# Kernel optimization log

Hardware: AMD Instinct MI355X
Metric: run time of the kernel (lower is better)

The kernel has to match this reference:

```python
import jax, jax.numpy as jnp
import numpy as np

CH_IN = 256
CA = CH_IN // 8   # attention channels (theta/phi)
CH = CH_IN // 2   # value channels (g)


def _maxpool2(t):
    # 2x2 max pool, stride 2: (B,C,H,W) -> (B,C,H//2,W//2)
    b, c, h, w = t.shape
    return t.reshape(b, c, h // 2, 2, w // 2, 2).max(axis=(3, 5))


def setup_inputs() -> dict:
    key = jax.random.key(0)
    ks = jax.random.split(key, 6)
    B, H, W = 16, 64, 64
    x = jax.random.normal(ks[0], (B, CH_IN, H, W), dtype=jnp.float32)
    # 1x1 conv weights stored as (out_ch, in_ch); spectral_norm is a weight
    # reparameterization, so the forward math is a plain conv with these weights.
    s = 0.05
    w_theta = jax.random.normal(ks[1], (CA, CH_IN), dtype=jnp.float32) * s
    w_phi = jax.random.normal(ks[2], (CA, CH_IN), dtype=jnp.float32) * s
    w_g = jax.random.normal(ks[3], (CH, CH_IN), dtype=jnp.float32) * s
    w_o = jax.random.normal(ks[4], (CH_IN, CH), dtype=jnp.float32) * s
    # gamma is initialized to 0 in the module; use a nonzero value so the
    # attention branch contributes to the output.
    gamma = jnp.asarray(0.5, dtype=jnp.float32)
    return {"x": x, "w_theta": w_theta, "w_phi": w_phi, "w_g": w_g,
            "w_o": w_o, "gamma": gamma}


def reference(x, w_theta, w_phi, w_g, w_o, gamma):
    B, C, H, W = x.shape
    # 1x1 convs as channel contractions
    theta = jnp.einsum('oc,bchw->bohw', w_theta, x)            # (B,CA,H,W)
    phi = _maxpool2(jnp.einsum('oc,bchw->bohw', w_phi, x))     # (B,CA,H/2,W/2)
    g = _maxpool2(jnp.einsum('oc,bchw->bohw', w_g, x))         # (B,CH,H/2,W/2)
    N = H * W
    M = N // 4
    theta = theta.reshape(B, CA, N)
    phi = phi.reshape(B, CA, M)
    g = g.reshape(B, CH, M)
    # beta = softmax(theta^T phi) over keys (no scaling, as in original)
    beta = jax.nn.softmax(jnp.einsum('bcn,bcm->bnm', theta, phi), axis=-1)  # (B,N,M)
    o = jnp.einsum('bcm,bnm->bcn', g, beta).reshape(B, CH, H, W)
    o = jnp.einsum('oc,bchw->bohw', w_o, o)                    # (B,C,H,W)
    return gamma * o + x
```

## Files before the change

kernel.cpp:

```cpp
#include <hip/hip_runtime.h>
#include <hip/hip_bf16.h>

#define NB 16
#define CIN 256
#define CA 32
#define CH 128
#define NN 4096
#define MM 1024

typedef __attribute__((ext_vector_type(8))) short s16x8;
typedef __attribute__((ext_vector_type(4))) float f32x4;

static __device__ __forceinline__ unsigned short f2bf(float x) {
  __hip_bfloat16 h = __float2bfloat16(x);
  return __builtin_bit_cast(unsigned short, h);
}
static __device__ __forceinline__ float bf2f(unsigned short u) {
  unsigned int v = ((unsigned int)u) << 16;
  return __builtin_bit_cast(float, v);
}
static __device__ __forceinline__ unsigned int pk2(float a, float b) {
  return (unsigned)f2bf(a) | ((unsigned)f2bf(b) << 16);
}
static __device__ __forceinline__ unsigned int pk2t(float a, float b) {
  return (__builtin_bit_cast(unsigned int, a) >> 16) |
         (__builtin_bit_cast(unsigned int, b) & 0xffff0000u);
}
static __device__ __forceinline__ void gload_lds16(const void* g, void* s) {
  __builtin_amdgcn_global_load_lds(
      (const __attribute__((address_space(1))) unsigned int*)g,
      (__attribute__((address_space(3))) unsigned int*)s, 16, 0, 0);
}

__global__ __launch_bounds__(256) void k_wcvt(const float* __restrict__ w_theta,
                                              const float* __restrict__ w_phi,
                                              const float* __restrict__ w_g,
                                              const float* __restrict__ w_o,
                                              unsigned short* __restrict__ wcat2,
                                              unsigned short* __restrict__ wo2) {
  const int i = blockIdx.x * 256 + threadIdx.x;
  if (i < 49152) {
    const int row = i >> 8, c = i & 255;
    const float v = (row < 32) ? w_theta[i]
                  : (row < 64) ? w_phi[i - 8192]
                               : w_g[i - 16384];
    const int dst = ((row >> 4) * 8 + (c >> 5)) * 512 +
                    (((c >> 3) & 3) * 16 + (row & 15)) * 8 + (c & 7);
    wcat2[dst] = f2bf(v);
  } else {
    const int w = i - 49152;
    const int c_out = w >> 7, k = w & 127;
    const int grp = (k >> 2) & 3;
    const int j = (((k >> 4) & 1) << 2) | (k & 3);
    const int dst = ((c_out >> 4) * 16 + (k >> 5) * 4 + grp) * 128 +
                    ((c_out & 15) << 3) + j;
    wo2[dst] = f2bf(w_o[w]);
  }
}

__global__ __launch_bounds__(512) void k_proj(const float* __restrict__ x,
                                              const unsigned short* __restrict__ wcat2,
                                              unsigned short* __restrict__ theta,
                                              unsigned short* __restrict__ phi2,
                                              unsigned short* __restrict__ g2) {
  __shared__ unsigned short lds[192 * 136];
  unsigned short (*xl)[32][132] = reinterpret_cast<unsigned short(*)[32][132]>(lds);
  unsigned short (*ol)[136] = reinterpret_cast<unsigned short(*)[136]>(lds);
  const int b = blockIdx.y;
  const int t = blockIdx.x;
  const int tid = threadIdx.x;
  const int wv = tid >> 6;
  const int l = tid & 63;
  const int grp = l >> 4, col = l & 15;
  const float* xb = x + (size_t)b * CIN * NN;
  const int cl0 = tid >> 5, nq0 = tid & 31;
  const int cl1 = (tid + 512) >> 5, nq1 = tid & 31;
  float4 ra0, ra1;
  auto LOADX = [&](int kc) {
    ra0 = *reinterpret_cast<const float4*>(xb + (size_t)(kc * 32 + cl0) * NN + t * 128 + nq0 * 4);
    ra1 = *reinterpret_cast<const float4*>(xb + (size_t)(kc * 32 + cl1) * NN + t * 128 + nq1 * 4);
  };
  auto WRITEX = [&](int buf) {
    *reinterpret_cast<uint2*>(&xl[buf][cl0][nq0 * 4]) =
        make_uint2(pk2(ra0.x, ra0.y), pk2(ra0.z, ra0.w));
    *reinterpret_cast<uint2*>(&xl[buf][cl1][nq1 * 4]) =
        make_uint2(pk2(ra1.x, ra1.y), pk2(ra1.z, ra1.w));
  };
  f32x4 acc[12];
#pragma unroll
  for (int r = 0; r < 12; ++r) acc[r] = f32x4{0.f, 0.f, 0.f, 0.f};
  LOADX(0);
  WRITEX(0);
  LOADX(1);
#pragma unroll 1
  for (int kc = 0; kc < 8; ++kc) {
    __syncthreads();
    if (kc < 7) {
      WRITEX((kc + 1) & 1);
      if (kc < 6) LOADX(kc + 2);
    }
    const int cur = kc & 1;
    s16x8 bfrag;
#pragma unroll
    for (int j = 0; j < 8; ++j)
      bfrag[j] = (short)xl[cur][grp * 8 + j][wv * 16 + col];
#pragma unroll
    for (int r = 0; r < 12; ++r) {
      const s16x8 af = *reinterpret_cast<const s16x8*>(
          wcat2 + (size_t)(r * 8 + kc) * 512 + l * 8);
      acc[r] = __builtin_amdgcn_mfma_f32_16x16x32_bf16(af, bfrag, acc[r], 0, 0, 0);
    }
  }
  __syncthreads();
#pragma unroll
  for (int r = 0; r < 12; ++r)
#pragma unroll
    for (int q = 0; q < 4; ++q)
      ol[r * 16 + grp * 4 + q][wv * 16 + col] = f2bf(acc[r][q]);
  __syncthreads();
  unsigned short* thb = theta + (size_t)b * NN * CA;
  for (int i = tid; i < 128 * 16; i += 512) {
    const int n = i >> 4, cp = (i & 15) << 1;
    const unsigned int v = (unsigned)ol[cp][n] | ((unsigned)ol[cp + 1][n] << 16);
    *reinterpret_cast<unsigned int*>(thb + (size_t)(t * 128 + n) * CA + cp) = v;
  }
  unsigned short* phb2 = phi2 + (size_t)b * MM * CA;
  for (int i = tid; i < 32 * 32; i += 512) {
    const int ca = i & 31, mx = i >> 5;
    const float v = fmaxf(
        fmaxf(bf2f(ol[32 + ca][2 * mx]), bf2f(ol[32 + ca][2 * mx + 1])),
        fmaxf(bf2f(ol[32 + ca][64 + 2 * mx]), bf2f(ol[32 + ca][64 + 2 * mx + 1])));
    const int m = t * 32 + mx;
    phb2[(m >> 4) * 512 + (ca >> 3) * 128 + (m & 15) * 8 + (ca & 7)] = f2bf(v);
  }
  unsigned short* gb2 = g2 + (size_t)b * CH * MM;
  for (int i = tid; i < 128 * 32; i += 512) {
    const int mx = i & 31, c = i >> 5;
    const float v = fmaxf(
        fmaxf(bf2f(ol[64 + c][2 * mx]), bf2f(ol[64 + c][2 * mx + 1])),
        fmaxf(bf2f(ol[64 + c][64 + 2 * mx]), bf2f(ol[64 + c][64 + 2 * mx + 1])));
    const int pg = (mx & 15) >> 2;
    const int pj = (mx & 3) | ((mx >> 4) << 2);
    gb2[(size_t)(t * 8 + (c >> 4)) * 512 + pg * 128 + (c & 15) * 8 + pj] = f2bf(v);
  }
}

__global__ __launch_bounds__(512, 4) void k_attn_out(
    const unsigned short* __restrict__ theta, const unsigned short* __restrict__ phi2,
    const unsigned short* __restrict__ g2, const unsigned short* __restrict__ wo2,
    const float* __restrict__ x, const float* __restrict__ gammap,
    float* __restrict__ out) {
  __shared__ __align__(16) unsigned short kv[2][10240];
  const int b = blockIdx.y;
  const int tid = threadIdx.x;
  const int wv = tid >> 6;
  const int l = tid & 63;
  const int grp = l >> 4, col = l & 15;
  const int n0 = blockIdx.x * 128 + wv * 16;
  const unsigned short* thb = theta + (size_t)b * NN * CA;
  const unsigned short* ph2b = phi2 + (size_t)b * MM * CA;
  const unsigned short* gb2 = g2 + (size_t)b * CH * MM;
  const s16x8 qf = *reinterpret_cast<const s16x8*>(thb + (size_t)(n0 + col) * CA + grp * 8);

  auto STAGE = [&](int buf, int tile) {
    const int mc = tile * 64;
    const unsigned short* ksrc = ph2b + (mc >> 4) * 512;
    const unsigned short* vsrc = gb2 + (size_t)(mc >> 5) * 4096;
#pragma unroll
    for (int q = 0; q < 3; ++q) {
      const int i = wv + q * 8;
      if (i < 20) {
        const unsigned short* src = (i < 4) ? (ksrc + i * 512) : (vsrc + (size_t)(i - 4) * 512);
        gload_lds16(src + (size_t)l * 8, &kv[buf][i * 512]);
      }
    }
  };

  f32x4 oa[8];
#pragma unroll
  for (int t = 0; t < 8; ++t) oa[t] = f32x4{0.f, 0.f, 0.f, 0.f};
  float m0 = 0.f, ls = 0.f;
  const f32x4 z4 = {0.f, 0.f, 0.f, 0.f};

  STAGE(0, 0);
  __syncthreads();
#pragma unroll 1
  for (int it = 0; it < 16; ++it) {
    const int cur = it & 1;
    if (it < 15) STAGE(cur ^ 1, it + 1);
    const unsigned short* kb = &kv[cur][0];
    const unsigned short* vb = &kv[cur][2048];
    const int fo = grp * 128 + col * 8;
    const s16x8 kf0 = *reinterpret_cast<const s16x8*>(kb + 0 * 512 + fo);
    const s16x8 kf1 = *reinterpret_cast<const s16x8*>(kb + 1 * 512 + fo);
    const s16x8 kf2 = *reinterpret_cast<const s16x8*>(kb + 2 * 512 + fo);
    const s16x8 kf3 = *reinterpret_cast<const s16x8*>(kb + 3 * 512 + fo);
    f32x4 s0 = __builtin_amdgcn_mfma_f32_16x16x32_bf16(kf0, qf, z4, 0, 0, 0);
    f32x4 s1 = __builtin_amdgcn_mfma_f32_16x16x32_bf16(kf1, qf, z4, 0, 0, 0);
    f32x4 s2 = __builtin_amdgcn_mfma_f32_16x16x32_bf16(kf2, qf, z4, 0, 0, 0);
    f32x4 s3 = __builtin_amdgcn_mfma_f32_16x16x32_bf16(kf3, qf, z4, 0, 0, 0);
    if (it == 0) {
      float cm = -INFINITY;
#pragma unroll
      for (int r = 0; r < 4; ++r)
        cm = fmaxf(cm, fmaxf(fmaxf(s0[r], s1[r]), fmaxf(s2[r], s3[r])));
      cm = fmaxf(cm, __shfl_xor(cm, 16));
      cm = fmaxf(cm, __shfl_xor(cm, 32));
      m0 = cm;
    }
    float p0[4], p1[4], p2[4], p3[4];
    float cs = 0.f;
#pragma unroll
    for (int r = 0; r < 4; ++r) {
      p0[r] = __expf(s0[r] - m0);
      p1[r] = __expf(s1[r] - m0);
      p2[r] = __expf(s2[r] - m0);
      p3[r] = __expf(s3[r] - m0);
      cs += (p0[r] + p1[r]) + (p2[r] + p3[r]);
    }
    ls += cs;
    const uint4 ua = make_uint4(pk2t(p0[0], p0[1]), pk2t(p0[2], p0[3]),
                                pk2t(p1[0], p1[1]), pk2t(p1[2], p1[3]));
    const uint4 ub = make_uint4(pk2t(p2[0], p2[1]), pk2t(p2[2], p2[3]),
                                pk2t(p3[0], p3[1]), pk2t(p3[2], p3[3]));
    const s16x8 pfA = __builtin_bit_cast(s16x8, ua);
    const s16x8 pfB = __builtin_bit_cast(s16x8, ub);
#pragma unroll
    for (int t = 0; t < 8; ++t) {
      const s16x8 vfA = *reinterpret_cast<const s16x8*>(vb + t * 512 + fo);
      const s16x8 vfB = *reinterpret_cast<const s16x8*>(vb + 4096 + t * 512 + fo);
      oa[t] = __builtin_amdgcn_mfma_f32_16x16x32_bf16(vfA, pfA, oa[t], 0, 0, 0);
      oa[t] = __builtin_amdgcn_mfma_f32_16x16x32_bf16(vfB, pfB, oa[t], 0, 0, 0);
    }
    __syncthreads();
  }
  ls += __shfl_xor(ls, 16);
  ls += __shfl_xor(ls, 32);
  const float ri = 1.f / ls;
  s16x8 of[4];
#pragma unroll
  for (int ks = 0; ks < 4; ++ks) {
    const uint4 u = make_uint4(
        pk2t(oa[2 * ks][0] * ri, oa[2 * ks][1] * ri),
        pk2t(oa[2 * ks][2] * ri, oa[2 * ks][3] * ri),
        pk2t(oa[2 * ks + 1][0] * ri, oa[2 * ks + 1][1] * ri),
        pk2t(oa[2 * ks + 1][2] * ri, oa[2 * ks + 1][3] * ri));
    of[ks] = __builtin_bit_cast(s16x8, u);
  }
  const float gamma = gammap[0];
  const float* xb2 = x + (size_t)b * CIN * NN;
  float* outb = out + (size_t)b * CIN * NN;
#pragma unroll 1
  for (int t2 = 0; t2 < 16; ++t2) {
    f32x4 a2 = {0.f, 0.f, 0.f, 0.f};
#pragma unroll
    for (int ks = 0; ks < 4; ++ks) {
      const s16x8 wf = *reinterpret_cast<const s16x8*>(
          wo2 + (size_t)(t2 * 16 + ks * 4 + grp) * 128 + col * 8);
      a2 = __builtin_amdgcn_mfma_f32_16x16x32_bf16(wf, of[ks], a2, 0, 0, 0);
    }
#pragma unroll
    for (int r = 0; r < 4; ++r) {
      const size_t idx = (size_t)(t2 * 16 + grp * 4 + r) * NN + n0 + col;
      outb[idx] = fmaf(gamma, a2[r], xb2[idx]);
    }
  }
}

extern "C" void kernel_launch(void* const* d_in, const int* in_sizes, int n_in,
                              void* d_out, int out_size, void* d_ws, size_t ws_size,
                              hipStream_t stream) {
  const float* x = (const float*)d_in[0];
  const float* w_theta = (const float*)d_in[1];
  const float* w_phi = (const float*)d_in[2];
  const float* w_g = (const float*)d_in[3];
  const float* w_o = (const float*)d_in[4];
  const float* gamma = (const float*)d_in[5];
  float* out = (float*)d_out;
  char* ws = (char*)d_ws;
  unsigned short* theta = (unsigned short*)(ws + 0);
  unsigned short* phi2 = (unsigned short*)(ws + 4194304);
  unsigned short* g2 = (unsigned short*)(ws + 5242880);
  unsigned short* wo2 = (unsigned short*)(ws + 9437184);
  unsigned short* wcat2 = (unsigned short*)(ws + 9502720);

  k_wcvt<<<dim3(320), 256, 0, stream>>>(w_theta, w_phi, w_g, w_o, wcat2, wo2);
  k_proj<<<dim3(NN / 128, NB), 512, 0, stream>>>(x, wcat2, theta, phi2, g2);
  k_attn_out<<<dim3(NN / 128, NB), 512, 0, stream>>>(theta, phi2, g2, wo2, x, gamma, out);
}
```

Before: 76.02 us.

## Process two query tiles per wave to reuse staged K/V fragments

Each wave now handles 32 query rows (two 16-row MFMA tiles) instead of 16, so every K/V fragment read from LDS feeds twice as many MFMAs. The grid is halved, which cuts global K/V staging traffic per query. In exchange, accumulator registers double, launch bounds drop to 2 blocks per CU, and only 256 blocks remain, which may reduce occupancy and latency hiding.

```diff
diff --git a/kernel.cpp b/kernel.cpp
--- a/kernel.cpp
+++ b/kernel.cpp
@@ -145,7 +145,7 @@
   }
 }
 
-__global__ __launch_bounds__(512, 4) void k_attn_out(
+__global__ __launch_bounds__(512, 2) void k_attn_out(
     const unsigned short* __restrict__ theta, const unsigned short* __restrict__ phi2,
     const unsigned short* __restrict__ g2, const unsigned short* __restrict__ wo2,
     const float* __restrict__ x, const float* __restrict__ gammap,
@@ -156,11 +156,12 @@
   const int wv = tid >> 6;
   const int l = tid & 63;
   const int grp = l >> 4, col = l & 15;
-  const int n0 = blockIdx.x * 128 + wv * 16;
+  const int n0 = blockIdx.x * 256 + wv * 32;
   const unsigned short* thb = theta + (size_t)b * NN * CA;
   const unsigned short* ph2b = phi2 + (size_t)b * MM * CA;
   const unsigned short* gb2 = g2 + (size_t)b * CH * MM;
-  const s16x8 qf = *reinterpret_cast<const s16x8*>(thb + (size_t)(n0 + col) * CA + grp * 8);
+  const s16x8 qf0 = *reinterpret_cast<const s16x8*>(thb + (size_t)(n0 + col) * CA + grp * 8);
+  const s16x8 qf1 = *reinterpret_cast<const s16x8*>(thb + (size_t)(n0 + 16 + col) * CA + grp * 8);
 
   auto STAGE = [&](int buf, int tile) {
     const int mc = tile * 64;
@@ -176,10 +177,13 @@
     }
   };
 
-  f32x4 oa[8];
-#pragma unroll
-  for (int t = 0; t < 8; ++t) oa[t] = f32x4{0.f, 0.f, 0.f, 0.f};
-  float m0 = 0.f, ls = 0.f;
+  f32x4 oa0[8], oa1[8];
+#pragma unroll
+  for (int t = 0; t < 8; ++t) {
+    oa0[t] = f32x4{0.f, 0.f, 0.f, 0.f};
+    oa1[t] = f32x4{0.f, 0.f, 0.f, 0.f};
+  }
+  float m0 = 0.f, ls0 = 0.f, ls1 = 0.f;
   const f32x4 z4 = {0.f, 0.f, 0.f, 0.f};
 
   STAGE(0, 0);
@@ -195,74 +199,115 @@
     const s16x8 kf1 = *reinterpret_cast<const s16x8*>(kb + 1 * 512 + fo);
     const s16x8 kf2 = *reinterpret_cast<const s16x8*>(kb + 2 * 512 + fo);
     const s16x8 kf3 = *reinterpret_cast<const s16x8*>(kb + 3 * 512 + fo);
-    f32x4 s0 = __builtin_amdgcn_mfma_f32_16x16x32_bf16(kf0, qf, z4, 0, 0, 0);
-    f32x4 s1 = __builtin_amdgcn_mfma_f32_16x16x32_bf16(kf1, qf, z4, 0, 0, 0);
-    f32x4 s2 = __builtin_amdgcn_mfma_f32_16x16x32_bf16(kf2, qf, z4, 0, 0, 0);
-    f32x4 s3 = __builtin_amdgcn_mfma_f32_16x16x32_bf16(kf3, qf, z4, 0, 0, 0);
+    f32x4 s00 = __builtin_amdgcn_mfma_f32_16x16x32_bf16(kf0, qf0, z4, 0, 0, 0);
+    f32x4 s01 = __builtin_amdgcn_mfma_f32_16x16x32_bf16(kf1, qf0, z4, 0, 0, 0);
+    f32x4 s02 = __builtin_amdgcn_mfma_f32_16x16x32_bf16(kf2, qf0, z4, 0, 0, 0);
+    f32x4 s03 = __builtin_amdgcn_mfma_f32_16x16x32_bf16(kf3, qf0, z4, 0, 0, 0);
+    f32x4 s10 = __builtin_amdgcn_mfma_f32_16x16x32_bf16(kf0, qf1, z4, 0, 0, 0);
+    f32x4 s11 = __builtin_amdgcn_mfma_f32_16x16x32_bf16(kf1, qf1, z4, 0, 0, 0);
+    f32x4 s12 = __builtin_amdgcn_mfma_f32_16x16x32_bf16(kf2, qf1, z4, 0, 0, 0);
+    f32x4 s13 = __builtin_amdgcn_mfma_f32_16x16x32_bf16(kf3, qf1, z4, 0, 0, 0);
     if (it == 0) {
       float cm = -INFINITY;
 #pragma unroll
-      for (int r = 0; r < 4; ++r)
-        cm = fmaxf(cm, fmaxf(fmaxf(s0[r], s1[r]), fmaxf(s2[r], s3[r])));
+      for (int r = 0; r < 4; ++r) {
+        cm = fmaxf(cm, fmaxf(fmaxf(s00[r], s01[r]), fmaxf(s02[r], s03[r])));
+        cm = fmaxf(cm, fmaxf(fmaxf(s10[r], s11[r]), fmaxf(s12[r], s13[r])));
+      }
       cm = fmaxf(cm, __shfl_xor(cm, 16));
       cm = fmaxf(cm, __shfl_xor(cm, 32));
       m0 = cm;
     }
-    float p0[4], p1[4], p2[4], p3[4];
-    float cs = 0.f;
-#pragma unroll
-    for (int r = 0; r < 4; ++r) {
-      p0[r] = __expf(s0[r] - m0);
-      p1[r] = __expf(s1[r] - m0);
-      p2[r] = __expf(s2[r] - m0);
-      p3[r] = __expf(s3[r] - m0);
-      cs += (p0[r] + p1[r]) + (p2[r] + p3[r]);
-    }
-    ls += cs;
-    const uint4 ua = make_uint4(pk2t(p0[0], p0[1]), pk2t(p0[2], p0[3]),
-                                pk2t(p1[0], p1[1]), pk2t(p1[2], p1[3]));
-    const uint4 ub = make_uint4(pk2t(p2[0], p2[1]), pk2t(p2[2], p2[3]),
-                                pk2t(p3[0], p3[1]), pk2t(p3[2], p3[3]));
-    const s16x8 pfA = __builtin_bit_cast(s16x8, ua);
-    const s16x8 pfB = __builtin_bit_cast(s16x8, ub);
+    s16x8 pfA0, pfB0, pfA1, pfB1;
+    {
+      float p0[4], p1[4], p2[4], p3[4];
+      float cs = 0.f;
+#pragma unroll
+      for (int r = 0; r < 4; ++r) {
+        p0[r] = __expf(s00[r] - m0);
+        p1[r] = __expf(s01[r] - m0);
+        p2[r] = __expf(s02[r] - m0);
+        p3[r] = __expf(s03[r] - m0);
+        cs += (p0[r] + p1[r]) + (p2[r] + p3[r]);
+      }
+      ls0 += cs;
+      const uint4 ua = make_uint4(pk2t(p0[0], p0[1]), pk2t(p0[2], p0[3]),
+                                  pk2t(p1[0], p1[1]), pk2t(p1[2], p1[3]));
+      const uint4 ub = make_uint4(pk2t(p2[0], p2[1]), pk2t(p2[2], p2[3]),
+                                  pk2t(p3[0], p3[1]), pk2t(p3[2], p3[3]));
+      pfA0 = __builtin_bit_cast(s16x8, ua);
+      pfB0 = __builtin_bit_cast(s16x8, ub);
+    }
+    {
+      float p0[4], p1[4], p2[4], p3[4];
+      float cs = 0.f;
+#pragma unroll
+      for (int r = 0; r < 4; ++r) {
+        p0[r] = __expf(s10[r] - m0);
+        p1[r] = __expf(s11[r] - m0);
+        p2[r] = __expf(s12[r] - m0);
+        p3[r] = __expf(s13[r] - m0);
+        cs += (p0[r] + p1[r]) + (p2[r] + p3[r]);
+      }
+      ls1 += cs;
+      const uint4 ua = make_uint4(pk2t(p0[0], p0[1]), pk2t(p0[2], p0[3]),
+                                  pk2t(p1[0], p1[1]), pk2t(p1[2], p1[3]));
+      const uint4 ub = make_uint4(pk2t(p2[0], p2[1]), pk2t(p2[2], p2[3]),
+                                  pk2t(p3[0], p3[1]), pk2t(p3[2], p3[3]));
+      pfA1 = __builtin_bit_cast(s16x8, ua);
+      pfB1 = __builtin_bit_cast(s16x8, ub);
+    }
 #pragma unroll
     for (int t = 0; t < 8; ++t) {
       const s16x8 vfA = *reinterpret_cast<const s16x8*>(vb + t * 512 + fo);
       const s16x8 vfB = *reinterpret_cast<const s16x8*>(vb + 4096 + t * 512 + fo);
-      oa[t] = __builtin_amdgcn_mfma_f32_16x16x32_bf16(vfA, pfA, oa[t], 0, 0, 0);
-      oa[t] = __builtin_amdgcn_mfma_f32_16x16x32_bf16(vfB, pfB, oa[t], 0, 0, 0);
+      oa0[t] = __builtin_amdgcn_mfma_f32_16x16x32_bf16(vfA, pfA0, oa0[t], 0, 0, 0);
+      oa0[t] = __builtin_amdgcn_mfma_f32_16x16x32_bf16(vfB, pfB0, oa0[t], 0, 0, 0);
+      oa1[t] = __builtin_amdgcn_mfma_f32_16x16x32_bf16(vfA, pfA1, oa1[t], 0, 0, 0);
+      oa1[t] = __builtin_amdgcn_mfma_f32_16x16x32_bf16(vfB, pfB1, oa1[t], 0, 0, 0);
     }
     __syncthreads();
   }
-  ls += __shfl_xor(ls, 16);
-  ls += __shfl_xor(ls, 32);
-  const float ri = 1.f / ls;
-  s16x8 of[4];
+  ls0 += __shfl_xor(ls0, 16);
+  ls0 += __shfl_xor(ls0, 32);
+  ls1 += __shfl_xor(ls1, 16);
+  ls1 += __shfl_xor(ls1, 32);
+  const float ri0 = 1.f / ls0, ri1 = 1.f / ls1;
+  s16x8 of0[4], of1[4];
 #pragma unroll
   for (int ks = 0; ks < 4; ++ks) {
-    const uint4 u = make_uint4(
-        pk2t(oa[2 * ks][0] * ri, oa[2 * ks][1] * ri),
-        pk2t(oa[2 * ks][2] * ri, oa[2 * ks][3] * ri),
-        pk2t(oa[2 * ks + 1][0] * ri, oa[2 * ks + 1][1] * ri),
-        pk2t(oa[2 * ks + 1][2] * ri, oa[2 * ks + 1][3] * ri));
-    of[ks] = __builtin_bit_cast(s16x8, u);
+    const uint4 u0 = make_uint4(
+        pk2t(oa0[2 * ks][0] * ri0, oa0[2 * ks][1] * ri0),
+        pk2t(oa0[2 * ks][2] * ri0, oa0[2 * ks][3] * ri0),
+        pk2t(oa0[2 * ks + 1][0] * ri0, oa0[2 * ks + 1][1] * ri0),
+        pk2t(oa0[2 * ks + 1][2] * ri0, oa0[2 * ks + 1][3] * ri0));
+    of0[ks] = __builtin_bit_cast(s16x8, u0);
+    const uint4 u1 = make_uint4(
+        pk2t(oa1[2 * ks][0] * ri1, oa1[2 * ks][1] * ri1),
+        pk2t(oa1[2 * ks][2] * ri1, oa1[2 * ks][3] * ri1),
+        pk2t(oa1[2 * ks + 1][0] * ri1, oa1[2 * ks + 1][1] * ri1),
+        pk2t(oa1[2 * ks + 1][2] * ri1, oa1[2 * ks + 1][3] * ri1));
+    of1[ks] = __builtin_bit_cast(s16x8, u1);
   }
   const float gamma = gammap[0];
   const float* xb2 = x + (size_t)b * CIN * NN;
   float* outb = out + (size_t)b * CIN * NN;
 #pragma unroll 1
   for (int t2 = 0; t2 < 16; ++t2) {
-    f32x4 a2 = {0.f, 0.f, 0.f, 0.f};
+    f32x4 a20 = {0.f, 0.f, 0.f, 0.f};
+    f32x4 a21 = {0.f, 0.f, 0.f, 0.f};
 #pragma unroll
     for (int ks = 0; ks < 4; ++ks) {
       const s16x8 wf = *reinterpret_cast<const s16x8*>(
           wo2 + (size_t)(t2 * 16 + ks * 4 + grp) * 128 + col * 8);
-      a2 = __builtin_amdgcn_mfma_f32_16x16x32_bf16(wf, of[ks], a2, 0, 0, 0);
+      a20 = __builtin_amdgcn_mfma_f32_16x16x32_bf16(wf, of0[ks], a20, 0, 0, 0);
+      a21 = __builtin_amdgcn_mfma_f32_16x16x32_bf16(wf, of1[ks], a21, 0, 0, 0);
     }
 #pragma unroll
     for (int r = 0; r < 4; ++r) {
       const size_t idx = (size_t)(t2 * 16 + grp * 4 + r) * NN + n0 + col;
-      outb[idx] = fmaf(gamma, a2[r], xb2[idx]);
+      outb[idx] = fmaf(gamma, a20[r], xb2[idx]);
+      outb[idx + 16] = fmaf(gamma, a21[r], xb2[idx + 16]);
     }
   }
 }
@@ -286,5 +331,5 @@
 
   k_wcvt<<<dim3(320), 256, 0, stream>>>(w_theta, w_phi, w_g, w_o, wcat2, wo2);
   k_proj<<<dim3(NN / 128, NB), 512, 0, stream>>>(x, wcat2, theta, phi2, g2);
-  k_attn_out<<<dim3(NN / 128, NB), 512, 0, stream>>>(theta, phi2, g2, wo2, x, gamma, out);
-}
+  k_attn_out<<<dim3(NN / 256, NB), 512, 0, stream>>>(theta, phi2, g2, wo2, x, gamma, out);
+}
```

Result: slower. 79.91 us (+5.1%).
